# Kernel tuning notes

Hardware: AMD Instinct MI355X
Metric: run time of the kernel (lower is better)

The kernel has to match this reference:

```python
import jax, jax.numpy as jnp
import numpy as np

N, D = 16384, 2048

def setup_inputs() -> dict:
    key = jax.random.key(0)
    k1, k2 = jax.random.split(key)
    cxr = jax.random.normal(k1, (N, D), dtype=jnp.float32)
    ehr = jax.random.normal(k2, (N, D), dtype=jnp.float32)
    return {"cxr": cxr, "ehr": ehr}

def reference(cxr, ehr):
    # Same math as diag(a_norm @ b_norm.T): row-wise cosine similarity.
    # a_norm = ehr / ||ehr||_row, b_norm = cxr / ||cxr||_row (L2 norms, dim=1)
    a_norm = ehr / jnp.linalg.norm(ehr, axis=1, keepdims=True)
    b_norm = cxr / jnp.linalg.norm(cxr, axis=1, keepdims=True)
    cos = jnp.sum(a_norm * b_norm, axis=1)  # [N] row-wise dot products
    return 1.0 - jnp.mean(cos)
```

## Files before the change

### kernel.cpp

```cpp
#include <hip/hip_runtime.h>
#include <hip/hip_bf16.h>


#define ROWS 16384
#define COLS 2048
#define BLOCK 256
#define WAVES_PER_BLOCK 4
#define GRID (ROWS / WAVES_PER_BLOCK)
#define NVEC (COLS / 4)
#define VPL (NVEC / 64)

__global__ __launch_bounds__(BLOCK) void cosine_partial_kernel(
    const float4* __restrict__ cxr,
    const float4* __restrict__ ehr,
    float* __restrict__ partial) {
    const int wave = threadIdx.x >> 6;
    const int lane = threadIdx.x & 63;
    const int row  = blockIdx.x * WAVES_PER_BLOCK + wave;

    const float4* __restrict__ a = cxr + (size_t)row * NVEC;
    const float4* __restrict__ b = ehr + (size_t)row * NVEC;

    float4 x[VPL], y[VPL];
    #pragma unroll
    for (int k = 0; k < VPL; ++k) x[k] = a[lane + 64 * k];
    #pragma unroll
    for (int k = 0; k < VPL; ++k) y[k] = b[lane + 64 * k];

    float dot = 0.f, aa = 0.f, bb = 0.f;
    #pragma unroll
    for (int k = 0; k < VPL; ++k) {
        dot += x[k].x * y[k].x + x[k].y * y[k].y + x[k].z * y[k].z + x[k].w * y[k].w;
        aa  += x[k].x * x[k].x + x[k].y * x[k].y + x[k].z * x[k].z + x[k].w * x[k].w;
        bb  += y[k].x * y[k].x + y[k].y * y[k].y + y[k].z * y[k].z + y[k].w * y[k].w;
    }

    #pragma unroll
    for (int off = 32; off > 0; off >>= 1) {
        dot += __shfl_down(dot, off, 64);
        aa  += __shfl_down(aa,  off, 64);
        bb  += __shfl_down(bb,  off, 64);
    }

    __shared__ float s_loss[WAVES_PER_BLOCK];
    if (lane == 0) {
        s_loss[wave] = 1.0f - dot * rsqrtf(aa * bb);
    }
    __syncthreads();
    if (threadIdx.x == 0) {
        partial[blockIdx.x] = s_loss[0] + s_loss[1] + s_loss[2] + s_loss[3];
    }
}

__global__ __launch_bounds__(BLOCK) void cosine_reduce_kernel(
    const float* __restrict__ partial,
    float* __restrict__ out) {
    float s = 0.f;
    for (int i = threadIdx.x; i < GRID; i += BLOCK) s += partial[i];
    #pragma unroll
    for (int off = 32; off > 0; off >>= 1) s += __shfl_down(s, off, 64);

    __shared__ float s_sum[BLOCK / 64];
    const int wave = threadIdx.x >> 6;
    const int lane = threadIdx.x & 63;
    if (lane == 0) s_sum[wave] = s;
    __syncthreads();
    if (threadIdx.x == 0) {
        out[0] = (s_sum[0] + s_sum[1] + s_sum[2] + s_sum[3]) * (1.0f / (float)ROWS);
    }
}

extern "C" void kernel_launch(void* const* d_in, const int* in_sizes, int n_in,
                              void* d_out, int out_size, void* d_ws, size_t ws_size,
                              hipStream_t stream) {
    const float4* cxr = (const float4*)d_in[0];
    const float4* ehr = (const float4*)d_in[1];
    float* out     = (float*)d_out;
    float* partial = (float*)d_ws;

    cosine_partial_kernel<<<GRID, BLOCK, 0, stream>>>(cxr, ehr, partial);
    cosine_reduce_kernel<<<1, BLOCK, 0, stream>>>(partial, out);
}
```

Baseline: 277.2 us.

## Process four rows per wave with double-buffered float4 loads

Each wave now computes cosine terms for four rows, streaming columns in 64-float4 steps with a two-stage register buffer so the next step's loads are issued before the current step's math. The grid shrinks to 1024 blocks, with a launch-bounds occupancy hint added. This aims to keep more loads in flight per wave and amortise per-wave overhead, at the cost of fewer total waves and more registers.

```diff
diff --git a/kernel.cpp b/kernel.cpp
--- a/kernel.cpp
+++ b/kernel.cpp
@@ -5,46 +5,72 @@
 #define ROWS 16384
 #define COLS 2048
 #define BLOCK 256
-#define WAVES_PER_BLOCK 4
-#define GRID (ROWS / WAVES_PER_BLOCK)
+#define GRID 1024
+#define RPW 4
 #define NVEC (COLS / 4)
-#define VPL (NVEC / 64)
+#define KSTEPS (NVEC / 64)
 
-__global__ __launch_bounds__(BLOCK) void cosine_partial_kernel(
+__global__ __launch_bounds__(BLOCK, 4) void cosine_partial_kernel(
     const float4* __restrict__ cxr,
     const float4* __restrict__ ehr,
     float* __restrict__ partial) {
     const int wave = threadIdx.x >> 6;
     const int lane = threadIdx.x & 63;
-    const int row  = blockIdx.x * WAVES_PER_BLOCK + wave;
+    const int wid  = blockIdx.x * (BLOCK / 64) + wave;
+    const int row0 = wid * RPW;
 
-    const float4* __restrict__ a = cxr + (size_t)row * NVEC;
-    const float4* __restrict__ b = ehr + (size_t)row * NVEC;
+    const float4* __restrict__ a0 = cxr + (size_t)row0 * NVEC + lane;
+    const float4* __restrict__ b0 = ehr + (size_t)row0 * NVEC + lane;
 
-    float4 x[VPL], y[VPL];
+    float dot[RPW], aa[RPW], bb[RPW];
     #pragma unroll
-    for (int k = 0; k < VPL; ++k) x[k] = a[lane + 64 * k];
+    for (int r = 0; r < RPW; ++r) { dot[r] = 0.f; aa[r] = 0.f; bb[r] = 0.f; }
+
+    float4 xb[2][RPW], yb[2][RPW];
     #pragma unroll
-    for (int k = 0; k < VPL; ++k) y[k] = b[lane + 64 * k];
+    for (int r = 0; r < RPW; ++r) {
+        xb[0][r] = a0[r * NVEC];
+        yb[0][r] = b0[r * NVEC];
+    }
 
-    float dot = 0.f, aa = 0.f, bb = 0.f;
     #pragma unroll
-    for (int k = 0; k < VPL; ++k) {
-        dot += x[k].x * y[k].x + x[k].y * y[k].y + x[k].z * y[k].z + x[k].w * y[k].w;
-        aa  += x[k].x * x[k].x + x[k].y * x[k].y + x[k].z * x[k].z + x[k].w * x[k].w;
-        bb  += y[k].x * y[k].x + y[k].y * y[k].y + y[k].z * y[k].z + y[k].w * y[k].w;
+    for (int k = 0; k < KSTEPS; ++k) {
+        const int cur = k & 1;
+        const int nxt = cur ^ 1;
+        if (k + 1 < KSTEPS) {
+            #pragma unroll
+            for (int r = 0; r < RPW; ++r) {
+                xb[nxt][r] = a0[r * NVEC + (k + 1) * 64];
+                yb[nxt][r] = b0[r * NVEC + (k + 1) * 64];
+            }
+        }
+        #pragma unroll
+        for (int r = 0; r < RPW; ++r) {
+            float4 x = xb[cur][r];
+            float4 y = yb[cur][r];
+            dot[r] += x.x * y.x + x.y * y.y + x.z * y.z + x.w * y.w;
+            aa[r]  += x.x * x.x + x.y * x.y + x.z * x.z + x.w * x.w;
+            bb[r]  += y.x * y.x + y.y * y.y + y.z * y.z + y.w * y.w;
+        }
     }
 
     #pragma unroll
     for (int off = 32; off > 0; off >>= 1) {
-        dot += __shfl_down(dot, off, 64);
-        aa  += __shfl_down(aa,  off, 64);
-        bb  += __shfl_down(bb,  off, 64);
+        #pragma unroll
+        for (int r = 0; r < RPW; ++r) {
+            dot[r] += __shfl_down(dot[r], off, 64);
+            aa[r]  += __shfl_down(aa[r],  off, 64);
+            bb[r]  += __shfl_down(bb[r],  off, 64);
+        }
     }
 
-    __shared__ float s_loss[WAVES_PER_BLOCK];
+    __shared__ float s_loss[BLOCK / 64];
     if (lane == 0) {
-        s_loss[wave] = 1.0f - dot * rsqrtf(aa * bb);
+        float loss = 0.f;
+        #pragma unroll
+        for (int r = 0; r < RPW; ++r)
+            loss += 1.0f - dot[r] * rsqrtf(aa[r] * bb[r]);
+        s_loss[wave] = loss;
     }
     __syncthreads();
     if (threadIdx.x == 0) {
```

Measured after the change: 288.5 us. 4.1% more time.

## Switch to persistent grid-strided blocks with software-prefetched row loads

Applied to the files above, without the earlier changes.

Replaces the one-row-per-wave layout with 512 persistent blocks, each walking 32 rows. Every thread loads one float4 per row and prefetches the next row's data while reducing the current one. Per-row partial sums are staged in shared memory and combined at the end. This cuts block count and reduce-kernel work, but lowers the number of loads in flight per thread and adds a full cross-wave reduction per row.

```diff
diff --git a/kernel.cpp b/kernel.cpp
--- a/kernel.cpp
+++ b/kernel.cpp
@@ -3,69 +3,86 @@
 
 
 #define ROWS 16384
-#define COLS 2048
-#define BLOCK 256
-#define WAVES_PER_BLOCK 4
-#define GRID (ROWS / WAVES_PER_BLOCK)
-#define NVEC (COLS / 4)
-#define VPL (NVEC / 64)
+#define COLS_V4 512
+#define BLOCK 512
+#define GRID 512
+#define STEPS (ROWS / GRID)
+#define WPB (BLOCK / 64)
 
-__global__ __launch_bounds__(BLOCK) void cosine_partial_kernel(
-    const float4* __restrict__ cxr,
-    const float4* __restrict__ ehr,
+__global__ __launch_bounds__(BLOCK, 2) void cosine_partial_kernel(
+    const float4* __restrict__ A,
+    const float4* __restrict__ B,
     float* __restrict__ partial) {
-    const int wave = threadIdx.x >> 6;
-    const int lane = threadIdx.x & 63;
-    const int row  = blockIdx.x * WAVES_PER_BLOCK + wave;
+    const int t    = threadIdx.x;
+    const int wave = t >> 6;
+    const int lane = t & 63;
 
-    const float4* __restrict__ a = cxr + (size_t)row * NVEC;
-    const float4* __restrict__ b = ehr + (size_t)row * NVEC;
+    __shared__ float s_part[STEPS][WPB][3];
 
-    float4 x[VPL], y[VPL];
-    #pragma unroll
-    for (int k = 0; k < VPL; ++k) x[k] = a[lane + 64 * k];
-    #pragma unroll
-    for (int k = 0; k < VPL; ++k) y[k] = b[lane + 64 * k];
+    const float4* __restrict__ a = A + (size_t)blockIdx.x * COLS_V4 + t;
+    const float4* __restrict__ b = B + (size_t)blockIdx.x * COLS_V4 + t;
+    const size_t stride = (size_t)GRID * COLS_V4;
 
-    float dot = 0.f, aa = 0.f, bb = 0.f;
-    #pragma unroll
-    for (int k = 0; k < VPL; ++k) {
-        dot += x[k].x * y[k].x + x[k].y * y[k].y + x[k].z * y[k].z + x[k].w * y[k].w;
-        aa  += x[k].x * x[k].x + x[k].y * x[k].y + x[k].z * x[k].z + x[k].w * x[k].w;
-        bb  += y[k].x * y[k].x + y[k].y * y[k].y + y[k].z * y[k].z + y[k].w * y[k].w;
-    }
-
-    #pragma unroll
-    for (int off = 32; off > 0; off >>= 1) {
-        dot += __shfl_down(dot, off, 64);
-        aa  += __shfl_down(aa,  off, 64);
-        bb  += __shfl_down(bb,  off, 64);
-    }
-
-    __shared__ float s_loss[WAVES_PER_BLOCK];
-    if (lane == 0) {
-        s_loss[wave] = 1.0f - dot * rsqrtf(aa * bb);
+    float4 x = a[0];
+    float4 y = b[0];
+    for (int s = 0; s < STEPS; ++s) {
+        float4 xn, yn;
+        if (s + 1 < STEPS) {
+            xn = a[(size_t)(s + 1) * stride];
+            yn = b[(size_t)(s + 1) * stride];
+        }
+        float d  = x.x * y.x + x.y * y.y + x.z * y.z + x.w * y.w;
+        float na = x.x * x.x + x.y * x.y + x.z * x.z + x.w * x.w;
+        float nb = y.x * y.x + y.y * y.y + y.z * y.z + y.w * y.w;
+        #pragma unroll
+        for (int off = 32; off > 0; off >>= 1) {
+            d  += __shfl_down(d,  off, 64);
+            na += __shfl_down(na, off, 64);
+            nb += __shfl_down(nb, off, 64);
+        }
+        if (lane == 0) {
+            s_part[s][wave][0] = d;
+            s_part[s][wave][1] = na;
+            s_part[s][wave][2] = nb;
+        }
+        x = xn;
+        y = yn;
     }
     __syncthreads();
-    if (threadIdx.x == 0) {
-        partial[blockIdx.x] = s_loss[0] + s_loss[1] + s_loss[2] + s_loss[3];
+
+    float loss = 0.f;
+    if (t < STEPS) {
+        float d = 0.f, na = 0.f, nb = 0.f;
+        #pragma unroll
+        for (int w = 0; w < WPB; ++w) {
+            d  += s_part[t][w][0];
+            na += s_part[t][w][1];
+            nb += s_part[t][w][2];
+        }
+        loss = 1.0f - d * rsqrtf(na * nb);
+    }
+    if (wave == 0) {
+        #pragma unroll
+        for (int off = 16; off > 0; off >>= 1)
+            loss += __shfl_down(loss, off, 64);
+        if (lane == 0) partial[blockIdx.x] = loss;
     }
 }
 
-__global__ __launch_bounds__(BLOCK) void cosine_reduce_kernel(
+__global__ __launch_bounds__(256) void cosine_reduce_kernel(
     const float* __restrict__ partial,
     float* __restrict__ out) {
-    float s = 0.f;
-    for (int i = threadIdx.x; i < GRID; i += BLOCK) s += partial[i];
+    const int t = threadIdx.x;
+    float s = partial[t] + partial[t + 256];
     #pragma unroll
     for (int off = 32; off > 0; off >>= 1) s += __shfl_down(s, off, 64);
 
-    __shared__ float s_sum[BLOCK / 64];
-    const int wave = threadIdx.x >> 6;
-    const int lane = threadIdx.x & 63;
+    __shared__ float s_sum[4];
+    const int wave = t >> 6;
+    const int lane = t & 63;
     if (lane == 0) s_sum[wave] = s;
     __syncthreads();
-    if (threadIdx.x == 0) {
+    if (t == 0) {
         out[0] = (s_sum[0] + s_sum[1] + s_sum[2] + s_sum[3]) * (1.0f / (float)ROWS);
     }
 }
@@ -79,5 +96,5 @@
     float* partial = (float*)d_ws;
 
     cosine_partial_kernel<<<GRID, BLOCK, 0, stream>>>(cxr, ehr, partial);
-    cosine_reduce_kernel<<<1, BLOCK, 0, stream>>>(partial, out);
+    cosine_reduce_kernel<<<1, 256, 0, stream>>>(partial, out);
 }
```

Measured after the change: 275.3 us. About the same (-0.7%).
